# Kernel tuning notes

Measured on AMD Instinct MI355X. Metric: run time of the kernel, lower is better.

The kernel has to match this reference:

```python
import jax, jax.numpy as jnp
import numpy as np

K = 3          # kernel_size
EPS = 1e-12    # epsilon from l2_normal and abs-clamp


def setup_inputs() -> dict:
    key = jax.random.key(0)
    k1, k2 = jax.random.split(key)
    B, H, W, C, F = 8, 224, 224, 32, 32
    image = jax.random.normal(k1, (B, H, W, C), dtype=jnp.float32)
    # glorot-uniform-ish weight, shape (1, C*K*K, filters)
    fan = C * K * K + F
    lim = np.sqrt(6.0 / fan).astype(np.float32)
    w = jax.random.uniform(k2, (1, C * K * K, F), dtype=jnp.float32, minval=-lim, maxval=lim)
    p = jnp.full((F,), 100.0 ** 0.5, dtype=jnp.float32)   # p init = sqrt(100)
    q = jnp.full((1,), 10.0 ** 0.5, dtype=jnp.float32)    # q init = sqrt(10)
    return {"image": image, "w": w, "p": p, "q": q}


def reference(image, w, p, q):
    # CosSim2D, kernel_size=3, stride=1, padding='same', non-depthwise.
    B, H, W, C = image.shape
    pad = K // 2
    padded = jnp.pad(image, ((0, 0), (pad, pad), (pad, pad), (0, 0)))
    # im2col: kernel-position-major, channel-minor -> matches tf.stack(axis=3) + reshape
    patches = jnp.stack(
        [padded[:, dy:dy + H, dx:dx + W, :] for dy in range(K) for dx in range(K)],
        axis=3,
    )  # (B, H, W, K*K, C)
    x = patches.reshape(B, H * W, K * K * C)
    q_term = jnp.square(q) / 10.0                       # scalar (broadcast)
    x_norm = jnp.sqrt(jnp.maximum(jnp.sum(x * x, axis=2, keepdims=True), EPS)) + q_term
    w_norm = jnp.sqrt(jnp.maximum(jnp.sum(w * w, axis=1, keepdims=True), EPS)) + q_term
    sim = jnp.matmul(x / x_norm, (w / w_norm)[0])       # (B, H*W, filters)
    out = jnp.sign(sim) * jnp.power(jnp.abs(sim) + EPS, jnp.square(p) / 100.0)
    return out.reshape(B, H, W, -1)
```

## Files before the change

kernel.cpp:

```cpp
#include <hip/hip_runtime.h>
#include <hip/hip_bf16.h>


#define H_ 224
#define W_ 224
#define C_ 32
#define F_ 32

#define NSTEP 18
#define HROWS 10
#define HCOLS 34
#define NPIX (HROWS * HCOLS)
#define NGRAN (NPIX * 8)
#define NGRAN_PAD 2816

typedef __bf16 bf16_t;
typedef bf16_t bf16x8 __attribute__((ext_vector_type(8)));
typedef float f32x16 __attribute__((ext_vector_type(16)));

#define WFRAG_BYTES (NSTEP * 64 * 8 * 2)

__device__ __forceinline__ void dma16(const void* gp, void* lp) {
  __builtin_amdgcn_global_load_lds(
      (const __attribute__((address_space(1))) void*)gp,
      (__attribute__((address_space(3))) void*)lp, 16, 0, 0);
}

__global__ __launch_bounds__(256) void cos2d_prep(
    const float* __restrict__ w, const float* __restrict__ p,
    const float* __restrict__ q, bf16_t* __restrict__ wfrag,
    float* __restrict__ winv, float* __restrict__ ef) {
  const int tid = threadIdx.x;
  if (blockIdx.x == 0) {
    __shared__ float part[8][32];
    const int f = tid & 31, kg = tid >> 5;
    float s = 0.f;
#pragma unroll
    for (int i = 0; i < 36; ++i) {
      const float v = w[(kg + 8 * i) * F_ + f];
      s += v * v;
    }
    part[kg][f] = s;
    __syncthreads();
    if (tid < 32) {
      float t = 0.f;
#pragma unroll
      for (int g = 0; g < 8; ++g) t += part[g][tid];
      const float qt = q[0] * q[0] * 0.1f;
      winv[tid] = 1.f / (sqrtf(fmaxf(t, 1e-12f)) + qt);
      ef[tid] = p[tid] * p[tid] * 0.01f;
    }
  } else {
    const int t = (blockIdx.x - 1) * 256 + tid;
    if (t < NSTEP * 64) {
      const int s2 = t >> 6, l = t & 63;
      const int ff = l & 31;
      union { bf16_t v[8]; uint4 u; } tv;
#pragma unroll
      for (int e = 0; e < 8; ++e) {
        const int kk = s2 * 16 + ((l >> 5) << 3) + e;
        tv.v[e] = (bf16_t)w[kk * F_ + ff];
      }
      *(uint4*)(wfrag + (size_t)t * 8) = tv.u;
    }
  }
}

__global__ __launch_bounds__(256, 3) void cos2d_main(
    const float* __restrict__ img, const bf16_t* __restrict__ wfrag,
    const float* __restrict__ winv, const float* __restrict__ ef,
    const float* __restrict__ q, float* __restrict__ out) {
  __shared__ __align__(16) float xt[NGRAN_PAD * 4];

  const int tid = threadIdx.x;
  const int lane = tid & 63;
  const int wv = tid >> 6;
  const int lp = lane & 31;
  const int hi2 = (lane >> 5) * 2;

  const int bid = blockIdx.x;
  const int tw = bid % 7;
  const int th = (bid / 7) % 28;
  const int b  = bid / 196;
  const int h0 = th * 8, w0 = tw * 32;

  const float qt = q[0] * q[0] * 0.1f;
  const float efv = ef[lp];
  const float wnv = winv[lp];
  const bool allfast = __all(__builtin_fabsf(efv - 1.0f) < 1e-6f);

  bf16x8 bfrag[NSTEP];
  const bf16x8* wf4 = (const bf16x8*)wfrag;
#pragma unroll
  for (int s2 = 0; s2 < NSTEP; ++s2) bfrag[s2] = wf4[s2 * 64 + lane];

#pragma unroll
  for (int k = 0; k < 11; ++k) {
    const int s = k * 256 + tid;
    float* lb = &xt[(k * 256 + wv * 64) * 4];
    if (s < NGRAN) {
      const int pp = s >> 3;
      const int c  = (s & 7) ^ (pp & 7);
      const int rr = pp / HCOLS, cc = pp - rr * HCOLS;
      const int hh = h0 - 1 + rr, wc = w0 - 1 + cc;
      if ((unsigned)hh < H_ && (unsigned)wc < W_) {
        dma16(img + ((size_t)(b * H_ + hh) * W_ + wc) * C_ + c * 4, lb);
      } else {
        *(float4*)&xt[(size_t)s * 4] = make_float4(0.f, 0.f, 0.f, 0.f);
      }
    }
  }
  __syncthreads();

  const int mr0 = wv * 2;

  f32x16 acc0, acc1;
#pragma unroll
  for (int i = 0; i < 16; ++i) { acc0[i] = 0.f; acc1[i] = 0.f; }
  float psum[4] = {0.f, 0.f, 0.f, 0.f};

#pragma unroll
  for (int h = 0; h < 2; ++h) {
#pragma unroll
    for (int dx = 0; dx < 3; ++dx) {
      const int c0 = h * 4 + hi2;
      bf16x8 af[4];
#pragma unroll
      for (int r = 0; r < 4; ++r) {
        const int p = (mr0 + r) * HCOLS + lp + dx;
        const int g0 = p * 8 + ((c0 + 0) ^ (p & 7));
        const int g1 = p * 8 + ((c0 + 1) ^ (p & 7));
        const float4 f0 = *(const float4*)&xt[(size_t)g0 * 4];
        const float4 f1 = *(const float4*)&xt[(size_t)g1 * 4];
        psum[r] += f0.x * f0.x + f0.y * f0.y + f0.z * f0.z + f0.w * f0.w +
                   f1.x * f1.x + f1.y * f1.y + f1.z * f1.z + f1.w * f1.w;
        bf16x8 a;
        a[0] = (bf16_t)f0.x; a[1] = (bf16_t)f0.y;
        a[2] = (bf16_t)f0.z; a[3] = (bf16_t)f0.w;
        a[4] = (bf16_t)f1.x; a[5] = (bf16_t)f1.y;
        a[6] = (bf16_t)f1.z; a[7] = (bf16_t)f1.w;
        af[r] = a;
      }
#pragma unroll
      for (int dy = 0; dy < 3; ++dy) {
        const bf16x8 bf = bfrag[2 * (dy * 3 + dx) + h];
        acc0 = __builtin_amdgcn_mfma_f32_32x32x16_bf16(af[dy],     bf, acc0, 0, 0, 0);
        acc1 = __builtin_amdgcn_mfma_f32_32x32x16_bf16(af[dy + 1], bf, acc1, 0, 0, 0);
      }
    }
  }

#pragma unroll
  for (int r = 0; r < 4; ++r) psum[r] += __shfl_xor(psum[r], 32);
  const float xn2_0 = psum[0] + psum[1] + psum[2];
  const float xn2_1 = psum[1] + psum[2] + psum[3];
  float xinv[2];
  xinv[0] = 1.f / (sqrtf(fmaxf(xn2_0, 1e-12f)) + qt);
  xinv[1] = 1.f / (sqrtf(fmaxf(xn2_1, 1e-12f)) + qt);

#pragma unroll
  for (int t = 0; t < 2; ++t) {
    const f32x16& acc = t ? acc1 : acc0;
    const int obase = (b * H_ + h0 + mr0 + t) * W_ + w0;
    if (allfast) {
#pragma unroll
      for (int jj = 0; jj < 16; ++jj) {
        const int row = (jj & 3) + 8 * (jj >> 2) + 4 * (lane >> 5);
        const float xi = __shfl(xinv[t], row);
        const float sim = acc[jj] * xi * wnv;
        const float r = copysignf(fabsf(sim) + 1e-12f, sim);
        __builtin_nontemporal_store(r, &out[(size_t)(obase + row) * F_ + lp]);
      }
    } else {
#pragma unroll
      for (int jj = 0; jj < 16; ++jj) {
        const int row = (jj & 3) + 8 * (jj >> 2) + 4 * (lane >> 5);
        const float xi = __shfl(xinv[t], row);
        const float sim = acc[jj] * xi * wnv;
        const float ps = fabsf(sim) + 1e-12f;
        float r = exp2f(efv * __log2f(ps));
        r = copysignf(r, sim);
        __builtin_nontemporal_store(r, &out[(size_t)(obase + row) * F_ + lp]);
      }
    }
  }
}

extern "C" void kernel_launch(void* const* d_in, const int* in_sizes, int n_in,
                              void* d_out, int out_size, void* d_ws, size_t ws_size,
                              hipStream_t stream) {
  const float* img = (const float*)d_in[0];
  const float* w   = (const float*)d_in[1];
  const float* p   = (const float*)d_in[2];
  const float* q   = (const float*)d_in[3];

  bf16_t* wfrag = (bf16_t*)d_ws;
  float*  winv  = (float*)((char*)d_ws + WFRAG_BYTES);
  float*  ef    = winv + 64;

  cos2d_prep<<<6, 256, 0, stream>>>(w, p, q, wfrag, winv, ef);
  cos2d_main<<<1568, 256, 0, stream>>>(img, wfrag, winv, ef, q, (float*)d_out);
}
```

Before: 32.67 us.

## Make main kernel persistent with double-buffered LDS staging of image tiles

Replaces the 1568 one-tile blocks with 256 persistent blocks. Each block walks tiles assigned per XCD and prefetches the next tile's halo into a second LDS buffer through global_load_lds while the current tile computes. Out-of-bounds halo chunks are now DMA'd from a zeroed pool in the workspace instead of being written with ds stores, so every lane issues a uniform count of loads and the vmcnt waits stay valid. The cost is doubled LDS per block, which lowers occupancy, plus reliance on hand-written waitcnt counts that must match the load count exactly.

```diff
diff --git a/kernel.cpp b/kernel.cpp
--- a/kernel.cpp
+++ b/kernel.cpp
@@ -13,6 +13,7 @@
 #define NPIX (HROWS * HCOLS)
 #define NGRAN (NPIX * 8)
 #define NGRAN_PAD 2816
+#define TPX 196
 
 typedef __bf16 bf16_t;
 typedef bf16_t bf16x8 __attribute__((ext_vector_type(8)));
@@ -29,7 +30,8 @@
 __global__ __launch_bounds__(256) void cos2d_prep(
     const float* __restrict__ w, const float* __restrict__ p,
     const float* __restrict__ q, bf16_t* __restrict__ wfrag,
-    float* __restrict__ winv, float* __restrict__ ef) {
+    float* __restrict__ winv, float* __restrict__ ef,
+    float* __restrict__ zpool) {
   const int tid = threadIdx.x;
   if (blockIdx.x == 0) {
     __shared__ float part[8][32];
@@ -41,6 +43,7 @@
       s += v * v;
     }
     part[kg][f] = s;
+    zpool[tid] = 0.f;
     __syncthreads();
     if (tid < 32) {
       float t = 0.f;
@@ -66,11 +69,12 @@
   }
 }
 
-__global__ __launch_bounds__(256, 3) void cos2d_main(
+__global__ __launch_bounds__(256) void cos2d_main(
     const float* __restrict__ img, const bf16_t* __restrict__ wfrag,
     const float* __restrict__ winv, const float* __restrict__ ef,
-    const float* __restrict__ q, float* __restrict__ out) {
-  __shared__ __align__(16) float xt[NGRAN_PAD * 4];
+    const float* __restrict__ q, const float* __restrict__ zpool,
+    float* __restrict__ out) {
+  __shared__ __align__(16) float xt[2][NGRAN_PAD * 4];
 
   const int tid = threadIdx.x;
   const int lane = tid & 63;
@@ -78,111 +82,135 @@
   const int lp = lane & 31;
   const int hi2 = (lane >> 5) * 2;
 
-  const int bid = blockIdx.x;
-  const int tw = bid % 7;
-  const int th = (bid / 7) % 28;
-  const int b  = bid / 196;
-  const int h0 = th * 8, w0 = tw * 32;
-
   const float qt = q[0] * q[0] * 0.1f;
   const float efv = ef[lp];
   const float wnv = winv[lp];
   const bool allfast = __all(__builtin_fabsf(efv - 1.0f) < 1e-6f);
 
+  const int xcd = blockIdx.x & 7;
+  const int slot = blockIdx.x >> 3;
+
   bf16x8 bfrag[NSTEP];
   const bf16x8* wf4 = (const bf16x8*)wfrag;
 #pragma unroll
   for (int s2 = 0; s2 < NSTEP; ++s2) bfrag[s2] = wf4[s2 * 64 + lane];
 
-#pragma unroll
-  for (int k = 0; k < 11; ++k) {
-    const int s = k * 256 + tid;
-    float* lb = &xt[(k * 256 + wv * 64) * 4];
-    if (s < NGRAN) {
-      const int pp = s >> 3;
-      const int c  = (s & 7) ^ (pp & 7);
+  auto stage = [&](int tile, float* xbuf) {
+    const int tw = tile % 7, th = (tile / 7) % 28, b = tile / TPX;
+    const int h0 = th * 8, w0 = tw * 32;
+#pragma unroll
+    for (int k = 0; k < 11; ++k) {
+      const int s = k * 256 + tid;
+      float* lb = xbuf + (k * 256 + wv * 64) * 4;
+      const int sc = s < NGRAN ? s : 0;
+      const int pp = sc >> 3;
+      const int c  = (sc & 7) ^ (pp & 7);
       const int rr = pp / HCOLS, cc = pp - rr * HCOLS;
       const int hh = h0 - 1 + rr, wc = w0 - 1 + cc;
-      if ((unsigned)hh < H_ && (unsigned)wc < W_) {
-        dma16(img + ((size_t)(b * H_ + hh) * W_ + wc) * C_ + c * 4, lb);
+      const bool live = (s < NGRAN) & ((unsigned)hh < H_) & ((unsigned)wc < W_);
+      const float* src = live
+          ? img + ((size_t)(b * H_ + hh) * W_ + wc) * C_ + c * 4
+          : zpool + lane * 4;
+      dma16(src, lb);
+    }
+  };
+
+  auto compute = [&](int tile, const float* xbuf) {
+    const int tw = tile % 7, th = (tile / 7) % 28, b = tile / TPX;
+    const int h0 = th * 8, w0 = tw * 32;
+    const int mr0 = wv * 2;
+
+    f32x16 acc0, acc1;
+#pragma unroll
+    for (int i = 0; i < 16; ++i) { acc0[i] = 0.f; acc1[i] = 0.f; }
+    float psum[4] = {0.f, 0.f, 0.f, 0.f};
+
+#pragma unroll
+    for (int h = 0; h < 2; ++h) {
+#pragma unroll
+      for (int dx = 0; dx < 3; ++dx) {
+        const int c0 = h * 4 + hi2;
+        bf16x8 af[4];
+#pragma unroll
+        for (int r = 0; r < 4; ++r) {
+          const int p = (mr0 + r) * HCOLS + lp + dx;
+          const int g0 = p * 8 + ((c0 + 0) ^ (p & 7));
+          const int g1 = p * 8 + ((c0 + 1) ^ (p & 7));
+          const float4 f0 = *(const float4*)&xbuf[(size_t)g0 * 4];
+          const float4 f1 = *(const float4*)&xbuf[(size_t)g1 * 4];
+          psum[r] += f0.x * f0.x + f0.y * f0.y + f0.z * f0.z + f0.w * f0.w +
+                     f1.x * f1.x + f1.y * f1.y + f1.z * f1.z + f1.w * f1.w;
+          bf16x8 a;
+          a[0] = (bf16_t)f0.x; a[1] = (bf16_t)f0.y;
+          a[2] = (bf16_t)f0.z; a[3] = (bf16_t)f0.w;
+          a[4] = (bf16_t)f1.x; a[5] = (bf16_t)f1.y;
+          a[6] = (bf16_t)f1.z; a[7] = (bf16_t)f1.w;
+          af[r] = a;
+        }
+#pragma unroll
+        for (int dy = 0; dy < 3; ++dy) {
+          const bf16x8 bf = bfrag[2 * (dy * 3 + dx) + h];
+          acc0 = __builtin_amdgcn_mfma_f32_32x32x16_bf16(af[dy],     bf, acc0, 0, 0, 0);
+          acc1 = __builtin_amdgcn_mfma_f32_32x32x16_bf16(af[dy + 1], bf, acc1, 0, 0, 0);
+        }
+      }
+    }
+
+#pragma unroll
+    for (int r = 0; r < 4; ++r) psum[r] += __shfl_xor(psum[r], 32);
+    float xinv[2];
+    xinv[0] = 1.f / (sqrtf(fmaxf(psum[0] + psum[1] + psum[2], 1e-12f)) + qt);
+    xinv[1] = 1.f / (sqrtf(fmaxf(psum[1] + psum[2] + psum[3], 1e-12f)) + qt);
+
+#pragma unroll
+    for (int t = 0; t < 2; ++t) {
+      const f32x16& acc = t ? acc1 : acc0;
+      const int obase = (b * H_ + h0 + mr0 + t) * W_ + w0;
+      if (allfast) {
+#pragma unroll
+        for (int jj = 0; jj < 16; ++jj) {
+          const int row = (jj & 3) + 8 * (jj >> 2) + 4 * (lane >> 5);
+          const float xi = __shfl(xinv[t], row);
+          const float sim = acc[jj] * xi * wnv;
+          const float r = copysignf(fabsf(sim) + 1e-12f, sim);
+          __builtin_nontemporal_store(r, &out[(size_t)(obase + row) * F_ + lp]);
+        }
       } else {
-        *(float4*)&xt[(size_t)s * 4] = make_float4(0.f, 0.f, 0.f, 0.f);
+#pragma unroll
+        for (int jj = 0; jj < 16; ++jj) {
+          const int row = (jj & 3) + 8 * (jj >> 2) + 4 * (lane >> 5);
+          const float xi = __shfl(xinv[t], row);
+          const float sim = acc[jj] * xi * wnv;
+          const float ps = fabsf(sim) + 1e-12f;
+          float r = exp2f(efv * __log2f(ps));
+          r = copysignf(r, sim);
+          __builtin_nontemporal_store(r, &out[(size_t)(obase + row) * F_ + lp]);
+        }
       }
     }
-  }
-  __syncthreads();
-
-  const int mr0 = wv * 2;
-
-  f32x16 acc0, acc1;
-#pragma unroll
-  for (int i = 0; i < 16; ++i) { acc0[i] = 0.f; acc1[i] = 0.f; }
-  float psum[4] = {0.f, 0.f, 0.f, 0.f};
-
-#pragma unroll
-  for (int h = 0; h < 2; ++h) {
-#pragma unroll
-    for (int dx = 0; dx < 3; ++dx) {
-      const int c0 = h * 4 + hi2;
-      bf16x8 af[4];
-#pragma unroll
-      for (int r = 0; r < 4; ++r) {
-        const int p = (mr0 + r) * HCOLS + lp + dx;
-        const int g0 = p * 8 + ((c0 + 0) ^ (p & 7));
-        const int g1 = p * 8 + ((c0 + 1) ^ (p & 7));
-        const float4 f0 = *(const float4*)&xt[(size_t)g0 * 4];
-        const float4 f1 = *(const float4*)&xt[(size_t)g1 * 4];
-        psum[r] += f0.x * f0.x + f0.y * f0.y + f0.z * f0.z + f0.w * f0.w +
-                   f1.x * f1.x + f1.y * f1.y + f1.z * f1.z + f1.w * f1.w;
-        bf16x8 a;
-        a[0] = (bf16_t)f0.x; a[1] = (bf16_t)f0.y;
-        a[2] = (bf16_t)f0.z; a[3] = (bf16_t)f0.w;
-        a[4] = (bf16_t)f1.x; a[5] = (bf16_t)f1.y;
-        a[6] = (bf16_t)f1.z; a[7] = (bf16_t)f1.w;
-        af[r] = a;
-      }
-#pragma unroll
-      for (int dy = 0; dy < 3; ++dy) {
-        const bf16x8 bf = bfrag[2 * (dy * 3 + dx) + h];
-        acc0 = __builtin_amdgcn_mfma_f32_32x32x16_bf16(af[dy],     bf, acc0, 0, 0, 0);
-        acc1 = __builtin_amdgcn_mfma_f32_32x32x16_bf16(af[dy + 1], bf, acc1, 0, 0, 0);
-      }
-    }
-  }
-
-#pragma unroll
-  for (int r = 0; r < 4; ++r) psum[r] += __shfl_xor(psum[r], 32);
-  const float xn2_0 = psum[0] + psum[1] + psum[2];
-  const float xn2_1 = psum[1] + psum[2] + psum[3];
-  float xinv[2];
-  xinv[0] = 1.f / (sqrtf(fmaxf(xn2_0, 1e-12f)) + qt);
-  xinv[1] = 1.f / (sqrtf(fmaxf(xn2_1, 1e-12f)) + qt);
-
-#pragma unroll
-  for (int t = 0; t < 2; ++t) {
-    const f32x16& acc = t ? acc1 : acc0;
-    const int obase = (b * H_ + h0 + mr0 + t) * W_ + w0;
-    if (allfast) {
-#pragma unroll
-      for (int jj = 0; jj < 16; ++jj) {
-        const int row = (jj & 3) + 8 * (jj >> 2) + 4 * (lane >> 5);
-        const float xi = __shfl(xinv[t], row);
-        const float sim = acc[jj] * xi * wnv;
-        const float r = copysignf(fabsf(sim) + 1e-12f, sim);
-        __builtin_nontemporal_store(r, &out[(size_t)(obase + row) * F_ + lp]);
-      }
+  };
+
+  stage(xcd * TPX + slot, &xt[0][0]);
+  int cur = 0;
+  for (int tl = slot; tl < TPX; tl += 32) {
+    const int tile = xcd * TPX + tl;
+    const bool have_next = (tl + 32) < TPX;
+    if (have_next) stage(xcd * TPX + tl + 32, &xt[cur ^ 1][0]);
+
+    if (have_next) {
+      asm volatile("s_waitcnt vmcnt(11)" ::: "memory");
     } else {
-#pragma unroll
-      for (int jj = 0; jj < 16; ++jj) {
-        const int row = (jj & 3) + 8 * (jj >> 2) + 4 * (lane >> 5);
-        const float xi = __shfl(xinv[t], row);
-        const float sim = acc[jj] * xi * wnv;
-        const float ps = fabsf(sim) + 1e-12f;
-        float r = exp2f(efv * __log2f(ps));
-        r = copysignf(r, sim);
-        __builtin_nontemporal_store(r, &out[(size_t)(obase + row) * F_ + lp]);
-      }
-    }
+      asm volatile("s_waitcnt vmcnt(0)" ::: "memory");
+    }
+    __builtin_amdgcn_sched_barrier(0);
+    __builtin_amdgcn_s_barrier();
+    __builtin_amdgcn_sched_barrier(0);
+
+    compute(tile, &xt[cur][0]);
+
+    __builtin_amdgcn_s_barrier();
+    __builtin_amdgcn_sched_barrier(0);
+    cur ^= 1;
   }
 }
 
@@ -197,7 +225,9 @@
   bf16_t* wfrag = (bf16_t*)d_ws;
   float*  winv  = (float*)((char*)d_ws + WFRAG_BYTES);
   float*  ef    = winv + 64;
-
-  cos2d_prep<<<6, 256, 0, stream>>>(w, p, q, wfrag, winv, ef);
-  cos2d_main<<<1568, 256, 0, stream>>>(img, wfrag, winv, ef, q, (float*)d_out);
-}
+  float*  zpool = ef + 64;
+
+  cos2d_prep<<<6, 256, 0, stream>>>(w, p, q, wfrag, winv, ef, zpool);
+  cos2d_main<<<256, 256, 0, stream>>>(img, wfrag, winv, ef, q, zpool,
+                                      (float*)d_out);
+}
```

Measured after the change: 45.09 us. 1.38x slower.
